# Kernel tuning notes

Measured on AMD Instinct MI355X. Metric: run time of the kernel, lower is better.

The kernel has to match this reference:

```python
import jax, jax.numpy as jnp
import numpy as np
import math

B, T, C = 4, 2048, 1024
D_ATTN, N_HEAD = 1024, 16
HEAD = D_ATTN // N_HEAD


def setup_inputs() -> dict:
    key = jax.random.key(0)
    k1, k2, k3 = jax.random.split(key, 3)
    x = jax.random.normal(k1, (B, T, C), dtype=jnp.float32)
    mask = jnp.tril(jnp.ones((T, T), dtype=jnp.int32))  # causal mask, 0 = blocked
    W_qkv = jax.random.normal(k2, (C, 3 * D_ATTN), dtype=jnp.float32) * (1.0 / math.sqrt(C))
    b_qkv = jnp.zeros((3 * D_ATTN,), dtype=jnp.float32)
    W_out = jax.random.normal(k3, (D_ATTN, C), dtype=jnp.float32) * (1.0 / math.sqrt(D_ATTN))
    b_out = jnp.zeros((C,), dtype=jnp.float32)
    return {"x": x, "mask": mask, "W_qkv": W_qkv, "b_qkv": b_qkv, "W_out": W_out, "b_out": b_out}


def reference(x, mask, W_qkv, b_qkv, W_out, b_out):
    Bx, Tx, Cx = x.shape
    qkv = x @ W_qkv + b_qkv                      # [B, T, 3*d_attn]
    q, k, v = jnp.split(qkv, 3, axis=-1)
    # [B, T, d_attn] -> [B, H, T, head]
    q = q.reshape(Bx, Tx, N_HEAD, HEAD).transpose(0, 2, 1, 3)
    k = k.reshape(Bx, Tx, N_HEAD, HEAD).transpose(0, 2, 1, 3)
    v = v.reshape(Bx, Tx, N_HEAD, HEAD).transpose(0, 2, 1, 3)
    scale = 1.0 / math.sqrt(HEAD)
    scores = jnp.einsum('bhqd,bhkd->bhqk', q, k) * scale  # [B, H, T, T]
    scores = jnp.where(mask == 0, -jnp.inf, scores)
    att = jax.nn.softmax(scores, axis=-1)
    out = jnp.einsum('bhqk,bhkd->bhqd', att, v)           # [B, H, T, head]
    out = out.transpose(0, 2, 1, 3).reshape(Bx, Tx, D_ATTN)
    return out @ W_out + b_out
```

## Files before the change

### kernel.cpp

```cpp
#include <hip/hip_runtime.h>

#define B_    4
#define T_    2048
#define C_    1024
#define DATTN 1024
#define NHEAD 16
#define M_    (B_*T_)
#define NQKV  (3*DATTN)

typedef __bf16 bf16;
typedef bf16  bf16x8 __attribute__((ext_vector_type(8)));
typedef bf16  bf16x4 __attribute__((ext_vector_type(4)));
typedef short s16x4  __attribute__((ext_vector_type(4)));
typedef float f32x4  __attribute__((ext_vector_type(4)));
typedef unsigned short u16x8 __attribute__((ext_vector_type(8)));

#define NEGBIG (-1e30f)
#define QSCALE (0.125f * 1.44269504088896f)

typedef const __attribute__((address_space(1))) unsigned int* gas_u32;
typedef __attribute__((address_space(3))) unsigned int* las_u32;

static __device__ __forceinline__ f32x4 mfma16(bf16x4 a, bf16x4 b, f32x4 c) {
#if __has_builtin(__builtin_amdgcn_mfma_f32_16x16x16bf16_1k)
    return __builtin_amdgcn_mfma_f32_16x16x16bf16_1k(
        __builtin_bit_cast(s16x4, a), __builtin_bit_cast(s16x4, b), c, 0, 0, 0);
#else
    asm("v_mfma_f32_16x16x16_bf16 %0, %1, %2, %0" : "+v"(c) : "v"(a), "v"(b));
    return c;
#endif
}

static __device__ __forceinline__ bf16x4 pk4(float a, float b, float c, float d) {
    union { unsigned int u[2]; bf16x4 v; } r;
    asm("v_cvt_pk_bf16_f32 %0, %1, %2" : "=v"(r.u[0]) : "v"(a), "v"(b));
    asm("v_cvt_pk_bf16_f32 %0, %1, %2" : "=v"(r.u[1]) : "v"(c), "v"(d));
    return r.v;
}

__global__ void detect_dtype(const unsigned short* __restrict__ x, int* flag) {
    __shared__ int cnt;
    if (threadIdx.x == 0) cnt = 0;
    __syncthreads();
    int local = 0;
    for (int j = 0; j < 8; ++j) {
        u16x8 v = *(const u16x8*)&x[(j * 256 + threadIdx.x) * 8];
        for (int k = 0; k < 8; ++k)
            if ((v[k] & 0x7F80) == 0x7F80) ++local;
    }
    atomicAdd(&cnt, local);
    __syncthreads();
    if (threadIdx.x == 0) *flag = (cnt > 0) ? 1 : 0;
}

__global__ void prep_all(const void* __restrict__ x, bf16* __restrict__ x_bf,
                         const void* __restrict__ bq, const void* __restrict__ bo,
                         bf16* __restrict__ dq, bf16* __restrict__ do_,
                         const void* __restrict__ Wq, bf16* __restrict__ Wqt,
                         const void* __restrict__ Wo, bf16* __restrict__ Wot,
                         const int* __restrict__ flag) {
    __shared__ bf16 tile[32][33];
    const int bid = blockIdx.x;
    const int tid = threadIdx.x;
    const int f = *flag;

    if (bid < 4096) {
        int i = (bid * 256 + tid) * 8;
        if (f == 0) {
            *(bf16x8*)&x_bf[i] = *(const bf16x8*)((const bf16*)x + i);
        } else {
            const float* s = (const float*)x + i;
            f32x4 a = *(const f32x4*)s, b2 = *(const f32x4*)(s + 4);
            bf16x8 r;
            r[0] = (bf16)a[0]; r[1] = (bf16)a[1]; r[2] = (bf16)a[2]; r[3] = (bf16)a[3];
            r[4] = (bf16)b2[0]; r[5] = (bf16)b2[1]; r[6] = (bf16)b2[2]; r[7] = (bf16)b2[3];
            *(bf16x8*)&x_bf[i] = r;
        }
        return;
    }
    if (bid < 4112) {
        int i = (bid - 4096) * 256 + tid;
        if (i < NQKV) {
            float v = f ? ((const float*)bq)[i] : (float)((const bf16*)bq)[i];
            if (i < DATTN) v *= QSCALE;
            dq[i] = (bf16)v;
        } else if (i - NQKV < C_) {
            do_[i - NQKV] = f ? (bf16)((const float*)bo)[i - NQKV]
                              : ((const bf16*)bo)[i - NQKV];
        }
        return;
    }

    const void* src; bf16* dst; int R, C, c0, r0; float scale; int scale_cols;
    if (bid < 7184) {
        int id = bid - 4112;
        src = Wq; dst = Wqt; R = C_; C = NQKV;
        c0 = (id % (NQKV / 32)) * 32; r0 = (id / (NQKV / 32)) * 32;
        scale = QSCALE; scale_cols = DATTN;
    } else {
        int id = bid - 7184;
        src = Wo; dst = Wot; R = DATTN; C = C_;
        c0 = (id % (C_ / 32)) * 32; r0 = (id / (C_ / 32)) * 32;
        scale = 1.0f; scale_cols = 0;
    }
    const int tx = tid & 31, ty = tid >> 5;
    const float s = (c0 + tx < scale_cols) ? scale : 1.0f;
    for (int p = 0; p < 4; ++p) {
        int row = p * 8 + ty;
        size_t idx = (size_t)(r0 + row) * C + c0 + tx;
        float v = f ? ((const float*)src)[idx] : (float)((const bf16*)src)[idx];
        tile[row][tx] = (bf16)(v * s);
    }
    __syncthreads();
    for (int p = 0; p < 4; ++p) {
        int row = p * 8 + ty;
        dst[(size_t)(c0 + row) * R + r0 + tx] = tile[tx][row];
    }
}

template<typename TC>
__global__ __launch_bounds__(256) void gemm_bt(const bf16* __restrict__ A,
                                               const bf16* __restrict__ Bt,
                                               const bf16* __restrict__ bias,
                                               TC* __restrict__ Cc,
                                               int M, int N, int K,
                                               const int* __restrict__ flag, int want,
                                               bf16* __restrict__ vt) {
    if (flag && *flag != want) return;
    __shared__ __align__(16) bf16 As[128 * 64];
    __shared__ __align__(16) bf16 Bs[128 * 64];
    const int tid  = threadIdx.x;
    const int lane = tid & 63, wave = tid >> 6;
    const int quad = lane >> 4, l15 = lane & 15;
    const int wr = wave >> 1, wc = wave & 1;
    const int m0 = blockIdx.y * 128, n0 = blockIdx.x * 128;
    const int srow = lane >> 3;
    const int scol = ((lane & 7) ^ srow) * 8;
    const int l7x8 = (l15 & 7);

    f32x4 acc[4][4];
    for (int i = 0; i < 4; ++i)
        for (int j = 0; j < 4; ++j)
            acc[i][j] = f32x4{0.f, 0.f, 0.f, 0.f};

    for (int k0 = 0; k0 < K; k0 += 64) {
        for (int c = 0; c < 4; ++c) {
            int chunk = wave * 4 + c;
            int row = chunk * 8 + srow;
            __builtin_amdgcn_global_load_lds(
                (gas_u32)&A[(size_t)(m0 + row) * K + k0 + scol],
                (las_u32)&As[chunk * 512], 16, 0, 0);
            __builtin_amdgcn_global_load_lds(
                (gas_u32)&Bt[(size_t)(n0 + row) * K + k0 + scol],
                (las_u32)&Bs[chunk * 512], 16, 0, 0);
        }
        __syncthreads();
        for (int ks = 0; ks < 2; ++ks) {
            bf16x8 af[4], bfr[4];
            for (int i = 0; i < 4; ++i)
                af[i] = *(const bf16x8*)&As[(wr * 64 + i * 16 + l15) * 64 +
                                            (((ks * 4 + quad) ^ l7x8) * 8)];
            for (int j = 0; j < 4; ++j)
                bfr[j] = *(const bf16x8*)&Bs[(wc * 64 + j * 16 + l15) * 64 +
                                             (((ks * 4 + quad) ^ l7x8) * 8)];
            for (int i = 0; i < 4; ++i)
                for (int j = 0; j < 4; ++j)
                    acc[i][j] = __builtin_amdgcn_mfma_f32_16x16x32_bf16(af[i], bfr[j], acc[i][j], 0, 0, 0);
        }
        __syncthreads();
    }

    if (vt && n0 >= 2 * DATTN) {
        for (int i = 0; i < 4; ++i) {
            int row = m0 + wr * 64 + i * 16 + quad * 4;
            int batch = row >> 11, t = row & (T_ - 1);
            for (int j = 0; j < 4; ++j) {
                int cg = n0 + wc * 64 + j * 16 + l15;
                int vcol = cg - 2 * DATTN;
                int h = vcol >> 6, d = vcol & 63;
                float bv = (float)bias[cg];
                bf16x4 o;
                for (int r = 0; r < 4; ++r) o[r] = (bf16)(acc[i][j][r] + bv);
                *(bf16x4*)&vt[((size_t)(batch * 16 + h) * 64 + d) * T_ + t] = o;
            }
        }
        return;
    }

    for (int i = 0; i < 4; ++i) {
        int row = m0 + wr * 64 + i * 16 + quad * 4;
        for (int j = 0; j < 4; ++j) {
            int col = n0 + wc * 64 + j * 16 + l15;
            float bv = (float)bias[col];
            for (int r = 0; r < 4; ++r) {
                float v = acc[i][j][r] + bv;
                if constexpr (__is_same(TC, float)) Cc[(size_t)(row + r) * N + col] = v;
                else                                Cc[(size_t)(row + r) * N + col] = (bf16)v;
            }
        }
    }
}

__global__ __launch_bounds__(256, 4) void attn_fused8(const bf16* __restrict__ qkv,
                                                      const bf16* __restrict__ vt,
                                                      bf16* __restrict__ out) {
    __shared__ __align__(16) bf16 Ks[2][64 * 64];
    __shared__ __align__(16) bf16 Vs[2][64 * 64];
    const int tid  = threadIdx.x;
    const int lane = tid & 63, wave = tid >> 6;
    const int quad = lane >> 4, l15 = lane & 15;
    const int srow = lane >> 3;
    const int scol = ((lane & 7) ^ srow) * 8;
    const int l7   = l15 & 7;
    const int g0   = quad >> 1, h4 = (quad & 1) * 4;
    const int bh = blockIdx.x & 63;
    const int i  = blockIdx.x >> 6;
    const int b  = bh >> 4, h = bh & 15;
    const int lo = i, hi = 31 - i;
    const size_t rowbase = (size_t)b * T_;

    const size_t koff = (size_t)(wave * 16 + srow) * NQKV + scol;
    const size_t voff = (size_t)(wave * 16 + srow) * T_ + scol;
    const bf16* kp = qkv + rowbase * NQKV + DATTN + h * 64;
    const bf16* vp = vt + (size_t)bh * 64 * T_;

    auto stage = [&](const bf16* kq, const bf16* vq, int buf) {
        for (int p = 0; p < 2; ++p) {
            int chunk = wave * 2 + p;
            __builtin_amdgcn_global_load_lds(
                (gas_u32)(kq + koff + (size_t)p * 8 * NQKV),
                (las_u32)&Ks[buf][chunk * 512], 16, 0, 0);
            __builtin_amdgcn_global_load_lds(
                (gas_u32)(vq + voff + (size_t)p * 8 * T_),
                (las_u32)&Vs[buf][chunk * 512], 16, 0, 0);
        }
    };

    bf16x8 qf[2][2];
#pragma unroll
    for (int t = 0; t < 2; ++t) {
        int q0 = (t ? hi : lo) * 64;
        size_t r = rowbase + q0 + wave * 16 + l15;
        const bf16* p = &qkv[r * NQKV + h * 64];
        qf[t][0] = *(const bf16x8*)&p[quad * 8];
        qf[t][1] = *(const bf16x8*)&p[32 + quad * 8];
    }

    bf16x4 onesf;
#pragma unroll
    for (int j = 0; j < 4; ++j) onesf[j] = (bf16)1.0f;

    f32x4 oa[2][4];
    f32x4 lac[2];
#pragma unroll
    for (int t = 0; t < 2; ++t) {
        lac[t] = f32x4{0.f, 0.f, 0.f, 0.f};
        for (int c = 0; c < 4; ++c)
            oa[t][c] = f32x4{0.f, 0.f, 0.f, 0.f};
    }

    stage(kp, vp, 0);
    kp += (size_t)64 * NQKV;
    vp += 64;

    for (int kt = 0; kt <= hi; ++kt) {
        const int k0 = kt * 64;
        const bool act0 = (kt <= lo);
        const int buf = kt & 1;
        __syncthreads();
        if (kt < hi) {
            stage(kp, vp, buf ^ 1);
            kp += (size_t)64 * NQKV;
            vp += 64;
        }

        const bf16* Kb = Ks[buf];
        const bf16* Vb = Vs[buf];

        f32x4 s0[4], s1[4];
#pragma unroll
        for (int c = 0; c < 4; ++c) {
            s0[c] = f32x4{0.f, 0.f, 0.f, 0.f};
            s1[c] = f32x4{0.f, 0.f, 0.f, 0.f};
        }
#pragma unroll
        for (int ks = 0; ks < 2; ++ks)
#pragma unroll
            for (int c = 0; c < 4; ++c) {
                bf16x8 kf = *(const bf16x8*)&Kb[(c * 16 + l15) * 64 +
                                                (((ks * 4 + quad) ^ l7) * 8)];
                if (act0) s0[c] = __builtin_amdgcn_mfma_f32_16x16x32_bf16(kf, qf[0][ks], s0[c], 0, 0, 0);
                s1[c] = __builtin_amdgcn_mfma_f32_16x16x32_bf16(kf, qf[1][ks], s1[c], 0, 0, 0);
            }

        bf16x4 paf[2][4];
#pragma unroll
        for (int t = 0; t < 2; ++t) {
            if (t == 0 && !act0) continue;
            const int q0 = (t ? hi : lo) * 64;
            const bool diag = (kt == (t ? hi : lo));
            const int qa = q0 + wave * 16 + l15;
#pragma unroll
            for (int c = 0; c < 4; ++c) {
                const int keyb = k0 + c * 16 + quad * 4;
                float pr[4];
#pragma unroll
                for (int r = 0; r < 4; ++r) {
                    float v = t ? s1[c][r] : s0[c][r];
                    if (diag && keyb + r > qa) v = NEGBIG;
                    pr[r] = __builtin_amdgcn_exp2f(v);
                }
                paf[t][c] = pk4(pr[0], pr[1], pr[2], pr[3]);
            }
        }

#pragma unroll
        for (int c = 0; c < 4; ++c) {
            if (act0) lac[0] = mfma16(paf[0][c], onesf, lac[0]);
            lac[1] = mfma16(paf[1][c], onesf, lac[1]);
        }

#pragma unroll
        for (int c = 0; c < 4; ++c)
#pragma unroll
            for (int c2 = 0; c2 < 4; ++c2) {
                bf16x4 vf = *(const bf16x4*)&Vb[(c2 * 16 + l15) * 64 +
                                                (((2 * c + g0) ^ l7) * 8) + h4];
                if (act0) oa[0][c2] = mfma16(paf[0][c], vf, oa[0][c2]);
                oa[1][c2] = mfma16(paf[1][c], vf, oa[1][c2]);
            }
    }

#pragma unroll
    for (int t = 0; t < 2; ++t) {
        int q0 = (t ? hi : lo) * 64;
        float inv[4];
#pragma unroll
        for (int r = 0; r < 4; ++r) inv[r] = 1.f / lac[t][r];
        size_t r0 = rowbase + q0 + wave * 16 + quad * 4;
#pragma unroll
        for (int c2 = 0; c2 < 4; ++c2) {
            int col = h * 64 + c2 * 16 + l15;
#pragma unroll
            for (int r = 0; r < 4; ++r)
                out[(r0 + r) * (size_t)DATTN + col] = (bf16)(oa[t][c2][r] * inv[r]);
        }
    }
}

extern "C" void kernel_launch(void* const* d_in, const int* in_sizes, int n_in,
                              void* d_out, int out_size, void* d_ws, size_t ws_size,
                              hipStream_t stream) {
    const void* x     = d_in[0];
    const void* W_qkv = d_in[2];
    const void* b_qkv = d_in[3];
    const void* W_out = d_in[4];
    const void* b_out = d_in[5];

    char* ws = (char*)d_ws;
    int*  flag    = (int*)ws;
    bf16* qkv_buf = (bf16*)(ws + 256);
    bf16* Wqkv_t  = (bf16*)(ws + 256 + 50331648);
    bf16* Wout_t  = (bf16*)(ws + 256 + 56623104);
    bf16* att_buf = (bf16*)(ws + 256 + 58720256);
    bf16* vt_buf  = (bf16*)(ws + 256 + 75497472);
    bf16* x_bf    = (bf16*)(ws + 256 + 92274688);
    bf16* bq_bf   = (bf16*)(ws + 256 + 109051904);
    bf16* bo_bf   = (bf16*)(ws + 256 + 109058048);

    detect_dtype<<<1, 256, 0, stream>>>((const unsigned short*)x, flag);

    prep_all<<<8208, 256, 0, stream>>>(x, x_bf, b_qkv, b_out, bq_bf, bo_bf,
                                       W_qkv, Wqkv_t, W_out, Wout_t, flag);

    gemm_bt<bf16><<<dim3(NQKV / 128, M_ / 128), 256, 0, stream>>>(
        x_bf, Wqkv_t, bq_bf, qkv_buf, M_, NQKV, C_, nullptr, 0, vt_buf);

    attn_fused8<<<dim3(B_ * NHEAD * 16), 256, 0, stream>>>(qkv_buf, vt_buf, att_buf);

    gemm_bt<bf16 ><<<dim3(C_ / 128, M_ / 128), 256, 0, stream>>>(
        att_buf, Wout_t, bo_bf, (bf16*)d_out, M_, C_, DATTN, flag, 0, nullptr);
    gemm_bt<float><<<dim3(C_ / 128, M_ / 128), 256, 0, stream>>>(
        att_buf, Wout_t, bo_bf, (float*)d_out, M_, C_, DATTN, flag, 1, nullptr);
}
```

Measured before the change: 272.0 us.

## Fold dtype detection into prep, merge output GEMMs, add XCD-aware block remap

Removes the separate single-block dtype-detect launch by having every prep_all block redo the small detection scan locally, with one block writing the flag for later kernels. The two flag-gated output GEMM launches become one gemm_out kernel that picks the fp32 or bf16 store at runtime. Both GEMMs now use a 1D grid with the block index remapped across 8 groups, meant to keep neighbouring tiles on the same XCD for L2 reuse. The cost is a redundant 16KB scan in each of the 8208 prep blocks, plus a runtime branch in the output store.

Measured after the change: 277.0 us. About the same (+1.9%).

```diff
diff --git a/kernel.cpp b/kernel.cpp
--- a/kernel.cpp
+++ b/kernel.cpp
@@ -38,9 +38,9 @@
     return r.v;
 }
 
-__global__ void detect_dtype(const unsigned short* __restrict__ x, int* flag) {
-    __shared__ int cnt;
-    if (threadIdx.x == 0) cnt = 0;
+static __device__ __forceinline__ int block_detect(const unsigned short* __restrict__ x,
+                                                   int* cnt) {
+    if (threadIdx.x == 0) *cnt = 0;
     __syncthreads();
     int local = 0;
     for (int j = 0; j < 8; ++j) {
@@ -48,9 +48,9 @@
         for (int k = 0; k < 8; ++k)
             if ((v[k] & 0x7F80) == 0x7F80) ++local;
     }
-    atomicAdd(&cnt, local);
+    if (local) atomicAdd(cnt, local);
     __syncthreads();
-    if (threadIdx.x == 0) *flag = (cnt > 0) ? 1 : 0;
+    return (*cnt > 0) ? 1 : 0;
 }
 
 __global__ void prep_all(const void* __restrict__ x, bf16* __restrict__ x_bf,
@@ -58,11 +58,12 @@
                          bf16* __restrict__ dq, bf16* __restrict__ do_,
                          const void* __restrict__ Wq, bf16* __restrict__ Wqt,
                          const void* __restrict__ Wo, bf16* __restrict__ Wot,
-                         const int* __restrict__ flag) {
+                         int* __restrict__ flag) {
     __shared__ bf16 tile[32][33];
+    __shared__ int cnt;
     const int bid = blockIdx.x;
     const int tid = threadIdx.x;
-    const int f = *flag;
+    const int f = block_detect((const unsigned short*)x, &cnt);
 
     if (bid < 4096) {
         int i = (bid * 256 + tid) * 8;
@@ -79,6 +80,7 @@
         return;
     }
     if (bid < 4112) {
+        if (bid == 4096 && tid == 0) *flag = f;
         int i = (bid - 4096) * 256 + tid;
         if (i < NQKV) {
             float v = f ? ((const float*)bq)[i] : (float)((const bf16*)bq)[i];
@@ -118,22 +120,22 @@
     }
 }
 
-template<typename TC>
 __global__ __launch_bounds__(256) void gemm_bt(const bf16* __restrict__ A,
                                                const bf16* __restrict__ Bt,
                                                const bf16* __restrict__ bias,
-                                               TC* __restrict__ Cc,
+                                               bf16* __restrict__ Cc,
                                                int M, int N, int K,
-                                               const int* __restrict__ flag, int want,
                                                bf16* __restrict__ vt) {
-    if (flag && *flag != want) return;
     __shared__ __align__(16) bf16 As[128 * 64];
     __shared__ __align__(16) bf16 Bs[128 * 64];
     const int tid  = threadIdx.x;
     const int lane = tid & 63, wave = tid >> 6;
     const int quad = lane >> 4, l15 = lane & 15;
     const int wr = wave >> 1, wc = wave & 1;
-    const int m0 = blockIdx.y * 128, n0 = blockIdx.x * 128;
+    const int nbx = N >> 7;
+    const int cpx = gridDim.x >> 3;
+    const int wg  = (blockIdx.x & 7) * cpx + (blockIdx.x >> 3);
+    const int m0 = (wg / nbx) * 128, n0 = (wg % nbx) * 128;
     const int srow = lane >> 3;
     const int scol = ((lane & 7) ^ srow) * 8;
     const int l7x8 = (l15 & 7);
@@ -192,10 +194,74 @@
         for (int j = 0; j < 4; ++j) {
             int col = n0 + wc * 64 + j * 16 + l15;
             float bv = (float)bias[col];
+            for (int r = 0; r < 4; ++r)
+                Cc[(size_t)(row + r) * N + col] = (bf16)(acc[i][j][r] + bv);
+        }
+    }
+}
+
+__global__ __launch_bounds__(256) void gemm_out(const bf16* __restrict__ A,
+                                                const bf16* __restrict__ Bt,
+                                                const bf16* __restrict__ bias,
+                                                void* __restrict__ out,
+                                                int M, int N, int K,
+                                                const int* __restrict__ flag) {
+    __shared__ __align__(16) bf16 As[128 * 64];
+    __shared__ __align__(16) bf16 Bs[128 * 64];
+    const int tid  = threadIdx.x;
+    const int lane = tid & 63, wave = tid >> 6;
+    const int quad = lane >> 4, l15 = lane & 15;
+    const int wr = wave >> 1, wc = wave & 1;
+    const int nbx = N >> 7;
+    const int cpx = gridDim.x >> 3;
+    const int wg  = (blockIdx.x & 7) * cpx + (blockIdx.x >> 3);
+    const int m0 = (wg / nbx) * 128, n0 = (wg % nbx) * 128;
+    const int srow = lane >> 3;
+    const int scol = ((lane & 7) ^ srow) * 8;
+    const int l7x8 = (l15 & 7);
+    const int f = *flag;
+
+    f32x4 acc[4][4];
+    for (int i = 0; i < 4; ++i)
+        for (int j = 0; j < 4; ++j)
+            acc[i][j] = f32x4{0.f, 0.f, 0.f, 0.f};
+
+    for (int k0 = 0; k0 < K; k0 += 64) {
+        for (int c = 0; c < 4; ++c) {
+            int chunk = wave * 4 + c;
+            int row = chunk * 8 + srow;
+            __builtin_amdgcn_global_load_lds(
+                (gas_u32)&A[(size_t)(m0 + row) * K + k0 + scol],
+                (las_u32)&As[chunk * 512], 16, 0, 0);
+            __builtin_amdgcn_global_load_lds(
+                (gas_u32)&Bt[(size_t)(n0 + row) * K + k0 + scol],
+                (las_u32)&Bs[chunk * 512], 16, 0, 0);
+        }
+        __syncthreads();
+        for (int ks = 0; ks < 2; ++ks) {
+            bf16x8 af[4], bfr[4];
+            for (int i = 0; i < 4; ++i)
+                af[i] = *(const bf16x8*)&As[(wr * 64 + i * 16 + l15) * 64 +
+                                            (((ks * 4 + quad) ^ l7x8) * 8)];
+            for (int j = 0; j < 4; ++j)
+                bfr[j] = *(const bf16x8*)&Bs[(wc * 64 + j * 16 + l15) * 64 +
+                                             (((ks * 4 + quad) ^ l7x8) * 8)];
+            for (int i = 0; i < 4; ++i)
+                for (int j = 0; j < 4; ++j)
+                    acc[i][j] = __builtin_amdgcn_mfma_f32_16x16x32_bf16(af[i], bfr[j], acc[i][j], 0, 0, 0);
+        }
+        __syncthreads();
+    }
+
+    for (int i = 0; i < 4; ++i) {
+        int row = m0 + wr * 64 + i * 16 + quad * 4;
+        for (int j = 0; j < 4; ++j) {
+            int col = n0 + wc * 64 + j * 16 + l15;
+            float bv = (float)bias[col];
             for (int r = 0; r < 4; ++r) {
                 float v = acc[i][j][r] + bv;
-                if constexpr (__is_same(TC, float)) Cc[(size_t)(row + r) * N + col] = v;
-                else                                Cc[(size_t)(row + r) * N + col] = (bf16)v;
+                if (f) ((float*)out)[(size_t)(row + r) * N + col] = v;
+                else   ((bf16*)out)[(size_t)(row + r) * N + col] = (bf16)v;
             }
         }
     }
@@ -368,18 +434,14 @@
     bf16* bq_bf   = (bf16*)(ws + 256 + 109051904);
     bf16* bo_bf   = (bf16*)(ws + 256 + 109058048);
 
-    detect_dtype<<<1, 256, 0, stream>>>((const unsigned short*)x, flag);
-
     prep_all<<<8208, 256, 0, stream>>>(x, x_bf, b_qkv, b_out, bq_bf, bo_bf,
                                        W_qkv, Wqkv_t, W_out, Wout_t, flag);
 
-    gemm_bt<bf16><<<dim3(NQKV / 128, M_ / 128), 256, 0, stream>>>(
-        x_bf, Wqkv_t, bq_bf, qkv_buf, M_, NQKV, C_, nullptr, 0, vt_buf);
+    gemm_bt<<<dim3((NQKV / 128) * (M_ / 128)), 256, 0, stream>>>(
+        x_bf, Wqkv_t, bq_bf, qkv_buf, M_, NQKV, C_, vt_buf);
 
     attn_fused8<<<dim3(B_ * NHEAD * 16), 256, 0, stream>>>(qkv_buf, vt_buf, att_buf);
 
-    gemm_bt<bf16 ><<<dim3(C_ / 128, M_ / 128), 256, 0, stream>>>(
-        att_buf, Wout_t, bo_bf, (bf16*)d_out, M_, C_, DATTN, flag, 0, nullptr);
-    gemm_bt<float><<<dim3(C_ / 128, M_ / 128), 256, 0, stream>>>(
-        att_buf, Wout_t, bo_bf, (float*)d_out, M_, C_, DATTN, flag, 1, nullptr);
-}
+    gemm_out<<<dim3((C_ / 128) * (M_ / 128)), 256, 0, stream>>>(
+        att_buf, Wout_t, bo_bf, d_out, M_, C_, DATTN, flag);
+}
```
